# Performance work log

Hardware: AMD Instinct MI355X
Metric: run time of the kernel (lower is better)

The kernel has to match this reference:

```python
import jax, jax.numpy as jnp
import numpy as np

TOP_K = 2


def setup_inputs() -> dict:
    key = jax.random.key(0)
    ks = jax.random.split(key, 5)
    B, S, H, E, F = 4, 1024, 1024, 16, 4096
    scale = 0.02
    return {
        "input_tensor": jax.random.normal(ks[0], (B, S, H), dtype=jnp.float32),
        "Wg": scale * jax.random.normal(ks[1], (H, E), dtype=jnp.float32),
        "bg": jnp.zeros((E,), dtype=jnp.float32),
        "W1": scale * jax.random.normal(ks[2], (E, H, F), dtype=jnp.float32),
        "b1": jnp.zeros((E, F), dtype=jnp.float32),
        "W2": scale * jax.random.normal(ks[3], (E, F, H), dtype=jnp.float32),
        "b2": jnp.zeros((E, H), dtype=jnp.float32),
    }


def reference(input_tensor, Wg, bg, W1, b1, W2, b2):
    # Faithful to DualOutputMoE.forward_first_pass: the per-(b,s,k) Python loop
    # plus _weighted_sum collapses ALL token expert outputs into a single
    # [1,1,H] vector normalized by the total routing weight (= B*S).
    B, S, H = input_tensor.shape
    T = B * S
    E = Wg.shape[1]
    x = input_tensor.reshape(T, H)

    routing_scores = x @ Wg + bg                    # [T, E] (raw gate logits)
    top_v, top_i = jax.lax.top_k(routing_scores, TOP_K)
    top_w = jax.nn.softmax(top_v, axis=-1)          # per-token top-k weights

    # combine[t, e] = sum_k top_w[t, k] * 1[top_i[t, k] == e]
    combine = jnp.zeros((T, E), x.dtype).at[jnp.arange(T)[:, None], top_i].add(top_w)
    total_weight = top_w.sum()                      # matches python sum of .item()s

    def expert_step(acc, params):
        w1, bb1, w2, bb2, c = params                # c: [T] combine weights for this expert
        y = jax.nn.gelu(x @ w1 + bb1, approximate=False) @ w2 + bb2  # [T, H]
        return acc + c @ y, None

    acc0 = jnp.zeros((H,), x.dtype)
    acc, _ = jax.lax.scan(expert_step, acc0, (W1, b1, W2, b2, combine.T))
    first_output = (acc / total_weight).reshape(1, 1, H)
    return first_output
```

## Files before the change

### kernel.cpp

```cpp
#include <hip/hip_runtime.h>
#include <hip/hip_bf16.h>
#include <math.h>

typedef __bf16 bf16_t;
typedef __bf16 bf16x4 __attribute__((ext_vector_type(4)));
typedef __bf16 bf16x8 __attribute__((ext_vector_type(8)));
typedef float  f32x4  __attribute__((ext_vector_type(4)));

#define T_TOK 4096
#define H_DIM 1024
#define E_NUM 16
#define F_DIM 4096
#define CH_ROWS 128
#define CH_MAX  32

#define WS_E0     0
#define WS_E1     16384
#define WS_W0     32768
#define WS_W1     49152
#define WS_COUNTS 65536
#define WS_SUMW   65664
#define WS_XOFF   65792
#define WS_LIDX   131072
#define WS_LW     393216
#define WS_GPART  655360
#define WS_P2     655360
#define WS_G      9043968
#define WS_XE     9306112

#define AS_GLOBAL(p) ((const __attribute__((address_space(1))) void*)(p))
#define AS_LDS(p)    ((__attribute__((address_space(3))) void*)(p))

__global__ __launch_bounds__(64) void k_route(const float* __restrict__ x,
    const float* __restrict__ Wg, const float* __restrict__ bg,
    int* __restrict__ e0, int* __restrict__ e1,
    float* __restrict__ w0, float* __restrict__ w1)
{
    const int t = blockIdx.x;
    const int lane = threadIdx.x;
    const float* xr = x + (size_t)t * H_DIM;

    float s[E_NUM];
#pragma unroll
    for (int e = 0; e < E_NUM; ++e) s[e] = 0.f;

#pragma unroll
    for (int i = 0; i < 16; ++i) {
        const int h = i * 64 + lane;
        const float xv = xr[h];
        const float4* wr = (const float4*)(Wg + (size_t)h * E_NUM);
        float4 q0 = wr[0], q1 = wr[1], q2 = wr[2], q3 = wr[3];
        s[0] += xv*q0.x;  s[1] += xv*q0.y;  s[2] += xv*q0.z;  s[3] += xv*q0.w;
        s[4] += xv*q1.x;  s[5] += xv*q1.y;  s[6] += xv*q1.z;  s[7] += xv*q1.w;
        s[8] += xv*q2.x;  s[9] += xv*q2.y;  s[10]+= xv*q2.z;  s[11]+= xv*q2.w;
        s[12]+= xv*q3.x;  s[13]+= xv*q3.y;  s[14]+= xv*q3.z;  s[15]+= xv*q3.w;
    }
#pragma unroll
    for (int off = 32; off >= 1; off >>= 1) {
#pragma unroll
        for (int e = 0; e < E_NUM; ++e) s[e] += __shfl_xor(s[e], off);
    }
    if (lane == 0) {
#pragma unroll
        for (int e = 0; e < E_NUM; ++e) s[e] += bg[e];
        float b1v = -3e38f; int i1 = 0;
#pragma unroll
        for (int e = 0; e < E_NUM; ++e) { if (s[e] > b1v) { b1v = s[e]; i1 = e; } }
        float b2v = -3e38f; int i2 = 0;
#pragma unroll
        for (int e = 0; e < E_NUM; ++e) { if (e != i1 && s[e] > b2v) { b2v = s[e]; i2 = e; } }
        const float ex  = expf(b2v - b1v);
        const float inv = 1.f / (1.f + ex);
        e0[t] = i1; e1[t] = i2;
        w0[t] = inv; w1[t] = ex * inv;
    }
}

__global__ __launch_bounds__(64) void k_lists(const int* __restrict__ e0, const int* __restrict__ e1,
    const float* __restrict__ w0, const float* __restrict__ w1,
    int* __restrict__ lidx, float* __restrict__ lw,
    int* __restrict__ counts, float* __restrict__ sumw)
{
    const int e = blockIdx.x;
    const int lane = threadIdx.x;
    int cnt = 0; float sw = 0.f;
    for (int base = 0; base < T_TOK; base += 64) {
        const int t = base + lane;
        const bool m0 = (e0[t] == e);
        const bool m1 = (e1[t] == e);
        const bool m  = m0 | m1;
        const unsigned long long bal = __ballot(m);
        const int pos = cnt + __popcll(bal & ((1ull << lane) - 1ull));
        if (m) {
            const float w = m0 ? w0[t] : w1[t];
            lidx[e * T_TOK + pos] = t;
            lw[e * T_TOK + pos]   = w;
            sw += w;
        }
        cnt += __popcll(bal);
    }
#pragma unroll
    for (int off = 32; off >= 1; off >>= 1) sw += __shfl_xor(sw, off);
    if (lane == 0) { counts[e] = cnt; sumw[e] = sw; }
}

__global__ void k_scan(const int* __restrict__ counts, int* __restrict__ xoff) {
    if (threadIdx.x == 0) {
        int o = 0;
        for (int e = 0; e < E_NUM; ++e) { xoff[e] = o; o += (counts[e] + CH_ROWS - 1) & ~(CH_ROWS - 1); }
    }
}

__global__ __launch_bounds__(256) void k_gather(const float* __restrict__ x,
    const int* __restrict__ lidx, const int* __restrict__ counts,
    const int* __restrict__ xoff, bf16_t* __restrict__ Xe)
{
    const int chunk = blockIdx.x >> 2;
    const int part  = blockIdx.x & 3;
    const int e = blockIdx.y;
    const int cnt = counts[e];
    const int start = chunk * CH_ROWS;
    if (chunk && start >= cnt) return;
    const int tid = threadIdx.x;
    const size_t rbase = (size_t)xoff[e] + start;

    for (int it = part * 16; it < part * 16 + 16; ++it) {
        const int task = it * 256 + tid;
        const int rl   = task >> 7;
        const int sc   = task & 127;
        const int row  = start + rl;
        bf16x8 v8 = {};
        if (row < cnt) {
            const int tok = lidx[e * T_TOK + row];
            const int l   = (sc & 7) ^ (rl & 7);
            const int k   = (sc >> 3) * 64 + l * 8;
            const float4 a = *(const float4*)(x + (size_t)tok * H_DIM + k);
            const float4 b = *(const float4*)(x + (size_t)tok * H_DIM + k + 4);
            v8[0]=(bf16_t)a.x; v8[1]=(bf16_t)a.y; v8[2]=(bf16_t)a.z; v8[3]=(bf16_t)a.w;
            v8[4]=(bf16_t)b.x; v8[5]=(bf16_t)b.y; v8[6]=(bf16_t)b.z; v8[7]=(bf16_t)b.w;
        }
        *(bf16x8*)(Xe + (rbase + rl) * H_DIM + sc * 8) = v8;
    }
}

__global__ __launch_bounds__(256, 2) void k_expert(
    const float* __restrict__ W1, const float* __restrict__ b1,
    const bf16_t* __restrict__ Xe, const float* __restrict__ lw,
    const int* __restrict__ counts, const int* __restrict__ xoff,
    float* __restrict__ gpart)
{
    const int ftile = blockIdx.x;
    const int chunk = blockIdx.y;
    const int e     = blockIdx.z;
    const int cnt   = counts[e];
    const int start = chunk * CH_ROWS;
    if (chunk && start >= cnt) return;

    __shared__ __align__(16) bf16_t Alds[2][CH_ROWS * 64];
    __shared__ __align__(16) bf16_t Blds[2][128 * 72];
    __shared__ float w_s[CH_ROWS];
    __shared__ float b1_s[128];
    __shared__ float gred[2][128];

    const int tid  = threadIdx.x;
    const int lane = tid & 63;
    const int wid  = tid >> 6;
    const int wm   = wid & 1;
    const int wn   = wid >> 1;
    const int lr   = lane & 15;
    const int lg   = lane >> 4;

    if (tid < CH_ROWS) {
        const int r = start + tid;
        w_s[tid] = (r < cnt) ? lw[e * T_TOK + r] : 0.f;
    }
    if (tid < 128) b1_s[tid] = b1[(size_t)e * F_DIM + ftile * 128 + tid];

    f32x4 acc[4][4];
#pragma unroll
    for (int i = 0; i < 4; ++i)
#pragma unroll
        for (int j = 0; j < 4; ++j)
#pragma unroll
            for (int q = 0; q < 4; ++q) acc[i][j][q] = 0.f;

    const bf16_t* Asrc = Xe + ((size_t)xoff[e] + start) * H_DIM;
    const int bf_  = tid & 127;
    const int kh2  = tid >> 7;
    const float* W1p = W1 + (size_t)e * H_DIM * F_DIM + (size_t)ftile * 128 + bf_;

    float bvE[32], bvO[32];

#define ISSUE_A(T, BUFC) { \
    const int k0 = (T) * 64; \
    _Pragma("unroll") \
    for (int p = 0; p < 4; ++p) { \
        const int seg = wid * 4 + p; \
        const bf16_t* src = Asrc + (size_t)(seg * 8 + (lane >> 3)) * H_DIM + k0 + (lane & 7) * 8; \
        __builtin_amdgcn_global_load_lds(AS_GLOBAL(src), \
            AS_LDS((char*)&Alds[BUFC][0] + seg * 1024), 16, 0, 0); \
    } }

#define ISSUE_B(T, BV) { \
    const float* wp = W1p + (size_t)((T) * 64 + kh2 * 32) * F_DIM; \
    _Pragma("unroll") \
    for (int j = 0; j < 32; ++j) BV[j] = wp[(size_t)j * F_DIM]; }

#define WRITE_B(BUFC, BV) { \
    _Pragma("unroll") \
    for (int c = 0; c < 4; ++c) { \
        bf16x8 pk; \
        _Pragma("unroll") \
        for (int q = 0; q < 8; ++q) pk[q] = (bf16_t)BV[c * 8 + q]; \
        *(bf16x8*)&Blds[BUFC][bf_ * 72 + kh2 * 32 + c * 8] = pk; \
    } }

#define COMPUTE(BUFC) { \
    _Pragma("unroll") \
    for (int kh = 0; kh < 2; ++kh) { \
        bf16x8 af[4], bfr[4]; \
        _Pragma("unroll") \
        for (int mf = 0; mf < 4; ++mf) { \
            const int r = wm * 64 + mf * 16 + lr; \
            const int eoff = (kh * 32 + lg * 8) ^ ((r & 7) * 8); \
            af[mf] = *(const bf16x8*)&Alds[BUFC][r * 64 + eoff]; \
        } \
        _Pragma("unroll") \
        for (int nf = 0; nf < 4; ++nf) \
            bfr[nf] = *(const bf16x8*)&Blds[BUFC][(wn * 64 + nf * 16 + lr) * 72 + kh * 32 + lg * 8]; \
        _Pragma("unroll") \
        for (int mf = 0; mf < 4; ++mf) \
            _Pragma("unroll") \
            for (int nf = 0; nf < 4; ++nf) \
                acc[mf][nf] = __builtin_amdgcn_mfma_f32_16x16x32_bf16(af[mf], bfr[nf], acc[mf][nf], 0, 0, 0); \
    } }

#define SB0 __builtin_amdgcn_sched_barrier(0)

    ISSUE_A(0, 0); SB0;
    ISSUE_B(0, bvE); SB0;
    ISSUE_B(1, bvO); SB0;
    WRITE_B(0, bvE);
    asm volatile("s_waitcnt vmcnt(32) lgkmcnt(0)" ::: "memory");
    SB0; __builtin_amdgcn_s_barrier(); SB0;

#define KSTEP(T, CUR, NXT, BVISS, BVWR) { \
    if ((T) < 15) { ISSUE_A((T) + 1, NXT); } SB0; \
    if ((T) < 14) { ISSUE_B((T) + 2, BVISS); } SB0; \
    COMPUTE(CUR); \
    if ((T) < 15) { WRITE_B(NXT, BVWR); } \
    if ((T) < 14) { \
        asm volatile("s_waitcnt vmcnt(32) lgkmcnt(0)" ::: "memory"); \
    } else { \
        asm volatile("s_waitcnt vmcnt(0) lgkmcnt(0)" ::: "memory"); \
    } \
    SB0; __builtin_amdgcn_s_barrier(); SB0; }

    for (int th = 0; th < 8; ++th) {
        const int t0 = th * 2;
        KSTEP(t0,     0, 1, bvE, bvO);
        KSTEP(t0 + 1, 1, 0, bvO, bvE);
    }

    float gcol[4] = {0.f, 0.f, 0.f, 0.f};
#pragma unroll
    for (int nf = 0; nf < 4; ++nf) {
        const float bb = b1_s[wn * 64 + nf * 16 + lr];
#pragma unroll
        for (int mf = 0; mf < 4; ++mf) {
#pragma unroll
            for (int i = 0; i < 4; ++i) {
                const int row = wm * 64 + mf * 16 + lg * 4 + i;
                const float h  = acc[mf][nf][i] + bb;
                const float gl = 0.5f * h * (1.f + erff(h * 0.70710678118654752f));
                gcol[nf] += w_s[row] * gl;
            }
        }
    }
#pragma unroll
    for (int nf = 0; nf < 4; ++nf) {
        gcol[nf] += __shfl_xor(gcol[nf], 16);
        gcol[nf] += __shfl_xor(gcol[nf], 32);
    }
    if (lane < 16) {
#pragma unroll
        for (int nf = 0; nf < 4; ++nf) gred[wm][wn * 64 + nf * 16 + lane] = gcol[nf];
    }
    __syncthreads();
    if (tid < 128) {
        const float sum = gred[0][tid] + gred[1][tid];
        gpart[(size_t)(e * CH_MAX + chunk) * F_DIM + ftile * 128 + tid] = sum;
    }
#undef ISSUE_A
#undef ISSUE_B
#undef WRITE_B
#undef COMPUTE
#undef KSTEP
#undef SB0
}

__global__ __launch_bounds__(256) void k_redg(const float* __restrict__ gpart,
    const int* __restrict__ counts, float* __restrict__ g)
{
    const int e = blockIdx.y;
    const int f = blockIdx.x * 256 + threadIdx.x;
    const int nch = (counts[e] + CH_ROWS - 1) / CH_ROWS;
    float s = 0.f;
    for (int c = 0; c < nch; ++c)
        s += gpart[(size_t)(e * CH_MAX + c) * F_DIM + f];
    g[(size_t)e * F_DIM + f] = s;
}

__global__ __launch_bounds__(256) void k_out1(const float* __restrict__ g,
    const float* __restrict__ W2, float* __restrict__ p2)
{
    const int fc = blockIdx.x;
    const int e  = blockIdx.y;
    const int tid = threadIdx.x;
    __shared__ float gs[128];
    if (tid < 128) gs[tid] = g[(size_t)e * F_DIM + fc * 128 + tid];
    __syncthreads();
    const float* W2p = W2 + (size_t)e * F_DIM * H_DIM + (size_t)fc * 128 * H_DIM;
    float ax = 0.f, ay = 0.f, az = 0.f, aw = 0.f;
#pragma unroll 8
    for (int f = 0; f < 128; ++f) {
        const float gv = gs[f];
        const float4 wv = *(const float4*)(W2p + (size_t)f * H_DIM + tid * 4);
        ax += gv * wv.x; ay += gv * wv.y; az += gv * wv.z; aw += gv * wv.w;
    }
    float4 st; st.x = ax; st.y = ay; st.z = az; st.w = aw;
    *(float4*)(p2 + (size_t)(e * 32 + fc) * H_DIM + tid * 4) = st;
}

__global__ __launch_bounds__(256) void k_out2(const float* __restrict__ p2,
    const float* __restrict__ sumw, const float* __restrict__ b2, float* __restrict__ out)
{
    const int tid = threadIdx.x;
    const int hh  = tid & 31;
    const int seg = tid >> 5;
    const int h   = blockIdx.x * 32 + hh;
    float s = 0.f;
    for (int j = 0; j < 64; ++j)
        s += p2[(size_t)(seg * 64 + j) * H_DIM + h];
    __shared__ float red[8][33];
    red[seg][hh] = s;
    __syncthreads();
    if (tid < 32) {
        const int h2 = blockIdx.x * 32 + tid;
        float tot = 0.f;
#pragma unroll
        for (int q = 0; q < 8; ++q) tot += red[q][tid];
        float tw = 0.f, bias = 0.f;
#pragma unroll
        for (int e = 0; e < E_NUM; ++e) { tw += sumw[e]; bias += sumw[e] * b2[e * H_DIM + h2]; }
        out[h2] = (tot + bias) / tw;
    }
}

extern "C" void kernel_launch(void* const* d_in, const int* in_sizes, int n_in,
                              void* d_out, int out_size, void* d_ws, size_t ws_size,
                              hipStream_t stream) {
    const float* x  = (const float*)d_in[0];
    const float* Wg = (const float*)d_in[1];
    const float* bg = (const float*)d_in[2];
    const float* W1 = (const float*)d_in[3];
    const float* b1 = (const float*)d_in[4];
    const float* W2 = (const float*)d_in[5];
    const float* b2 = (const float*)d_in[6];
    float* out = (float*)d_out;

    char* ws = (char*)d_ws;
    int*    e0     = (int*)(ws + WS_E0);
    int*    e1     = (int*)(ws + WS_E1);
    float*  w0     = (float*)(ws + WS_W0);
    float*  w1     = (float*)(ws + WS_W1);
    int*    counts = (int*)(ws + WS_COUNTS);
    float*  sumw   = (float*)(ws + WS_SUMW);
    int*    xoff   = (int*)(ws + WS_XOFF);
    int*    lidx   = (int*)(ws + WS_LIDX);
    float*  lw     = (float*)(ws + WS_LW);
    float*  gpart  = (float*)(ws + WS_GPART);
    float*  g      = (float*)(ws + WS_G);
    float*  p2     = (float*)(ws + WS_P2);
    bf16_t* Xe     = (bf16_t*)(ws + WS_XE);

    k_route<<<T_TOK, 64, 0, stream>>>(x, Wg, bg, e0, e1, w0, w1);
    k_lists<<<E_NUM, 64, 0, stream>>>(e0, e1, w0, w1, lidx, lw, counts, sumw);
    k_scan<<<1, 64, 0, stream>>>(counts, xoff);
    k_gather<<<dim3(CH_MAX * 4, E_NUM), 256, 0, stream>>>(x, lidx, counts, xoff, Xe);
    k_expert<<<dim3(F_DIM / 128, CH_MAX, E_NUM), 256, 0, stream>>>(W1, b1, Xe, lw, counts, xoff, gpart);
    k_redg<<<dim3(F_DIM / 256, E_NUM), 256, 0, stream>>>(gpart, counts, g);
    k_out1<<<dim3(32, E_NUM), 256, 0, stream>>>(g, W2, p2);
    k_out2<<<32, 256, 0, stream>>>(p2, sumw, b2, out);
}
```

Baseline: 308.9 us.

## Pre-transpose W1 to swizzled bf16 tiles and stream both operands via LDS DMA

Adds a k_w1t kernel that converts each expert's W1 from fp32 into bf16 tiles laid out in 64x128 K-major blocks with an XOR swizzle. It also reorganizes the gathered Xe into contiguous tiled slabs. k_expert then loads both A and B operands with global_load_lds, replacing the strided per-thread fp32 W1 loads and register conversion, and uses a simpler double-buffered loop. The cost is an extra pass over W1 (read fp32, write bf16) plus a dependence on workspace size, which may force processing experts in batches.

Result: slower. 367.6 us (+19.0%).

```diff
diff --git a/kernel.cpp b/kernel.cpp
--- a/kernel.cpp
+++ b/kernel.cpp
@@ -27,6 +27,8 @@
 #define WS_P2     655360
 #define WS_G      9043968
 #define WS_XE     9306112
+#define WS_W1T    30277632
+#define W1T_PER_E 8388608
 
 #define AS_GLOBAL(p) ((const __attribute__((address_space(1))) void*)(p))
 #define AS_LDS(p)    ((__attribute__((address_space(3))) void*)(p))
@@ -115,49 +117,94 @@
     const int* __restrict__ lidx, const int* __restrict__ counts,
     const int* __restrict__ xoff, bf16_t* __restrict__ Xe)
 {
-    const int chunk = blockIdx.x >> 2;
-    const int part  = blockIdx.x & 3;
+    const int chunk = blockIdx.x >> 1;
+    const int part  = blockIdx.x & 1;
     const int e = blockIdx.y;
     const int cnt = counts[e];
     const int start = chunk * CH_ROWS;
     if (chunk && start >= cnt) return;
     const int tid = threadIdx.x;
-    const size_t rbase = (size_t)xoff[e] + start;
-
-    for (int it = part * 16; it < part * 16 + 16; ++it) {
-        const int task = it * 256 + tid;
-        const int rl   = task >> 7;
-        const int sc   = task & 127;
+    const size_t base = ((size_t)(xoff[e] >> 7) + chunk) * 131072;
+
+    for (int it = 0; it < 32; ++it) {
+        const int u    = part * 8192 + it * 256 + tid;
+        const int kt   = u >> 10;
+        const int wi   = u & 1023;
+        const int rl   = wi >> 3;
+        const int c    = wi & 7;
         const int row  = start + rl;
         bf16x8 v8 = {};
         if (row < cnt) {
             const int tok = lidx[e * T_TOK + row];
-            const int l   = (sc & 7) ^ (rl & 7);
-            const int k   = (sc >> 3) * 64 + l * 8;
+            const int cp  = c ^ (rl & 7);
+            const int k   = kt * 64 + cp * 8;
             const float4 a = *(const float4*)(x + (size_t)tok * H_DIM + k);
             const float4 b = *(const float4*)(x + (size_t)tok * H_DIM + k + 4);
             v8[0]=(bf16_t)a.x; v8[1]=(bf16_t)a.y; v8[2]=(bf16_t)a.z; v8[3]=(bf16_t)a.w;
             v8[4]=(bf16_t)b.x; v8[5]=(bf16_t)b.y; v8[6]=(bf16_t)b.z; v8[7]=(bf16_t)b.w;
         }
-        *(bf16x8*)(Xe + (rbase + rl) * H_DIM + sc * 8) = v8;
+        *(bf16x8*)(Xe + base + (size_t)kt * 8192 + rl * 64 + c * 8) = v8;
+    }
+}
+
+__global__ __launch_bounds__(512, 1) void k_w1t(const float* __restrict__ W1,
+    bf16_t* __restrict__ W1T, int ebase)
+{
+    const int kt = blockIdx.x;
+    const int fq = blockIdx.y;
+    const int ge = blockIdx.z;
+    const int e  = ebase + ge;
+    const int tid = threadIdx.x;
+
+    __shared__ bf16_t S[64][1024];
+
+    const float* src = W1 + (size_t)e * H_DIM * F_DIM + (size_t)(kt * 64) * F_DIM + fq * 1024;
+    for (int it = 0; it < 32; ++it) {
+        const int u   = it * 512 + tid;
+        const int row = u >> 8;
+        const int c4  = u & 255;
+        const float4 v = *(const float4*)(src + (size_t)row * F_DIM + c4 * 4);
+        bf16x4 b4; b4[0]=(bf16_t)v.x; b4[1]=(bf16_t)v.y; b4[2]=(bf16_t)v.z; b4[3]=(bf16_t)v.w;
+        *(bf16x4*)&S[row][c4 * 4] = b4;
+    }
+    __syncthreads();
+
+#pragma unroll
+    for (int ot = 0; ot < 2; ++ot) {
+        const int orow = ot * 512 + tid;
+        const int ftl  = orow >> 7;
+        const int f    = orow & 127;
+        const int fg   = ftl * 128 + f;
+        bf16_t kv[64];
+#pragma unroll
+        for (int k = 0; k < 64; ++k) kv[k] = S[k][fg];
+        bf16_t* dst = W1T + ((((size_t)ge * 32 + (fq * 8 + ftl)) * 16 + kt) * 8192) + f * 64;
+#pragma unroll
+        for (int j = 0; j < 8; ++j) {
+            bf16x8 pk;
+#pragma unroll
+            for (int q = 0; q < 8; ++q) pk[q] = kv[j * 8 + q];
+            *(bf16x8*)&dst[((j ^ (f & 7)) * 8)] = pk;
+        }
     }
 }
 
 __global__ __launch_bounds__(256, 2) void k_expert(
-    const float* __restrict__ W1, const float* __restrict__ b1,
+    const bf16_t* __restrict__ W1T, const float* __restrict__ b1,
     const bf16_t* __restrict__ Xe, const float* __restrict__ lw,
     const int* __restrict__ counts, const int* __restrict__ xoff,
-    float* __restrict__ gpart)
+    float* __restrict__ gpart, int ebase)
 {
     const int ftile = blockIdx.x;
     const int chunk = blockIdx.y;
-    const int e     = blockIdx.z;
+    const int ge    = blockIdx.z;
+    const int e     = ebase + ge;
     const int cnt   = counts[e];
     const int start = chunk * CH_ROWS;
     if (chunk && start >= cnt) return;
 
-    __shared__ __align__(16) bf16_t Alds[2][CH_ROWS * 64];
-    __shared__ __align__(16) bf16_t Blds[2][128 * 72];
+    __shared__ __align__(16) bf16_t Alds[2][8192];
+    __shared__ __align__(16) bf16_t Blds[2][8192];
     __shared__ float w_s[CH_ROWS];
     __shared__ float b1_s[128];
     __shared__ float gred[2][128];
@@ -184,50 +231,33 @@
 #pragma unroll
             for (int q = 0; q < 4; ++q) acc[i][j][q] = 0.f;
 
-    const bf16_t* Asrc = Xe + ((size_t)xoff[e] + start) * H_DIM;
-    const int bf_  = tid & 127;
-    const int kh2  = tid >> 7;
-    const float* W1p = W1 + (size_t)e * H_DIM * F_DIM + (size_t)ftile * 128 + bf_;
-
-    float bvE[32], bvO[32];
-
-#define ISSUE_A(T, BUFC) { \
-    const int k0 = (T) * 64; \
+    const bf16_t* XeSlab = Xe + ((size_t)(xoff[e] >> 7) + chunk) * 131072;
+    const bf16_t* W1Slab = W1T + (((size_t)ge * 32 + ftile) * 16) * 8192;
+
+#define STAGE(T, BUF) { \
+    const bf16_t* sa = XeSlab + (size_t)(T) * 8192; \
+    const bf16_t* sb = W1Slab + (size_t)(T) * 8192; \
     _Pragma("unroll") \
     for (int p = 0; p < 4; ++p) { \
-        const int seg = wid * 4 + p; \
-        const bf16_t* src = Asrc + (size_t)(seg * 8 + (lane >> 3)) * H_DIM + k0 + (lane & 7) * 8; \
-        __builtin_amdgcn_global_load_lds(AS_GLOBAL(src), \
-            AS_LDS((char*)&Alds[BUFC][0] + seg * 1024), 16, 0, 0); \
+        const int off = p * 2048 + wid * 512; \
+        __builtin_amdgcn_global_load_lds(AS_GLOBAL(sa + off + lane * 8), AS_LDS(&Alds[BUF][off]), 16, 0, 0); \
+        __builtin_amdgcn_global_load_lds(AS_GLOBAL(sb + off + lane * 8), AS_LDS(&Blds[BUF][off]), 16, 0, 0); \
     } }
 
-#define ISSUE_B(T, BV) { \
-    const float* wp = W1p + (size_t)((T) * 64 + kh2 * 32) * F_DIM; \
-    _Pragma("unroll") \
-    for (int j = 0; j < 32; ++j) BV[j] = wp[(size_t)j * F_DIM]; }
-
-#define WRITE_B(BUFC, BV) { \
-    _Pragma("unroll") \
-    for (int c = 0; c < 4; ++c) { \
-        bf16x8 pk; \
-        _Pragma("unroll") \
-        for (int q = 0; q < 8; ++q) pk[q] = (bf16_t)BV[c * 8 + q]; \
-        *(bf16x8*)&Blds[BUFC][bf_ * 72 + kh2 * 32 + c * 8] = pk; \
-    } }
-
-#define COMPUTE(BUFC) { \
+#define COMPUTE(BUF) { \
     _Pragma("unroll") \
     for (int kh = 0; kh < 2; ++kh) { \
         bf16x8 af[4], bfr[4]; \
         _Pragma("unroll") \
         for (int mf = 0; mf < 4; ++mf) { \
             const int r = wm * 64 + mf * 16 + lr; \
-            const int eoff = (kh * 32 + lg * 8) ^ ((r & 7) * 8); \
-            af[mf] = *(const bf16x8*)&Alds[BUFC][r * 64 + eoff]; \
+            af[mf] = *(const bf16x8*)&Alds[BUF][r * 64 + (((kh << 2) | lg) ^ (r & 7)) * 8]; \
         } \
         _Pragma("unroll") \
-        for (int nf = 0; nf < 4; ++nf) \
-            bfr[nf] = *(const bf16x8*)&Blds[BUFC][(wn * 64 + nf * 16 + lr) * 72 + kh * 32 + lg * 8]; \
+        for (int nf = 0; nf < 4; ++nf) { \
+            const int f = wn * 64 + nf * 16 + lr; \
+            bfr[nf] = *(const bf16x8*)&Blds[BUF][f * 64 + (((kh << 2) | lg) ^ (f & 7)) * 8]; \
+        } \
         _Pragma("unroll") \
         for (int mf = 0; mf < 4; ++mf) \
             _Pragma("unroll") \
@@ -235,32 +265,20 @@
                 acc[mf][nf] = __builtin_amdgcn_mfma_f32_16x16x32_bf16(af[mf], bfr[nf], acc[mf][nf], 0, 0, 0); \
     } }
 
-#define SB0 __builtin_amdgcn_sched_barrier(0)
-
-    ISSUE_A(0, 0); SB0;
-    ISSUE_B(0, bvE); SB0;
-    ISSUE_B(1, bvO); SB0;
-    WRITE_B(0, bvE);
-    asm volatile("s_waitcnt vmcnt(32) lgkmcnt(0)" ::: "memory");
-    SB0; __builtin_amdgcn_s_barrier(); SB0;
-
-#define KSTEP(T, CUR, NXT, BVISS, BVWR) { \
-    if ((T) < 15) { ISSUE_A((T) + 1, NXT); } SB0; \
-    if ((T) < 14) { ISSUE_B((T) + 2, BVISS); } SB0; \
-    COMPUTE(CUR); \
-    if ((T) < 15) { WRITE_B(NXT, BVWR); } \
-    if ((T) < 14) { \
-        asm volatile("s_waitcnt vmcnt(32) lgkmcnt(0)" ::: "memory"); \
-    } else { \
-        asm volatile("s_waitcnt vmcnt(0) lgkmcnt(0)" ::: "memory"); \
-    } \
-    SB0; __builtin_amdgcn_s_barrier(); SB0; }
-
-    for (int th = 0; th < 8; ++th) {
-        const int t0 = th * 2;
-        KSTEP(t0,     0, 1, bvE, bvO);
-        KSTEP(t0 + 1, 1, 0, bvO, bvE);
-    }
+    STAGE(0, 0);
+    __syncthreads();
+
+    int cur = 0;
+#pragma unroll 2
+    for (int t = 0; t < 16; ++t) {
+        if (t < 15) { STAGE(t + 1, cur ^ 1); }
+        __builtin_amdgcn_sched_barrier(0);
+        COMPUTE(cur);
+        __syncthreads();
+        cur ^= 1;
+    }
+#undef STAGE
+#undef COMPUTE
 
     float gcol[4] = {0.f, 0.f, 0.f, 0.f};
 #pragma unroll
@@ -291,12 +309,6 @@
         const float sum = gred[0][tid] + gred[1][tid];
         gpart[(size_t)(e * CH_MAX + chunk) * F_DIM + ftile * 128 + tid] = sum;
     }
-#undef ISSUE_A
-#undef ISSUE_B
-#undef WRITE_B
-#undef COMPUTE
-#undef KSTEP
-#undef SB0
 }
 
 __global__ __launch_bounds__(256) void k_redg(const float* __restrict__ gpart,
@@ -383,12 +395,24 @@
     float*  g      = (float*)(ws + WS_G);
     float*  p2     = (float*)(ws + WS_P2);
     bf16_t* Xe     = (bf16_t*)(ws + WS_XE);
+    bf16_t* W1T    = (bf16_t*)(ws + WS_W1T);
+
+    int cap = 1;
+    if (ws_size > (size_t)WS_W1T + (size_t)W1T_PER_E) {
+        size_t c = (ws_size - (size_t)WS_W1T) / (size_t)W1T_PER_E;
+        cap = (c >= 16) ? 16 : (int)c;
+        if (cap < 1) cap = 1;
+    }
 
     k_route<<<T_TOK, 64, 0, stream>>>(x, Wg, bg, e0, e1, w0, w1);
     k_lists<<<E_NUM, 64, 0, stream>>>(e0, e1, w0, w1, lidx, lw, counts, sumw);
     k_scan<<<1, 64, 0, stream>>>(counts, xoff);
-    k_gather<<<dim3(CH_MAX * 4, E_NUM), 256, 0, stream>>>(x, lidx, counts, xoff, Xe);
-    k_expert<<<dim3(F_DIM / 128, CH_MAX, E_NUM), 256, 0, stream>>>(W1, b1, Xe, lw, counts, xoff, gpart);
+    k_gather<<<dim3(CH_MAX * 2, E_NUM), 256, 0, stream>>>(x, lidx, counts, xoff, Xe);
+    for (int eb = 0; eb < E_NUM; eb += cap) {
+        const int gN = (E_NUM - eb < cap) ? (E_NUM - eb) : cap;
+        k_w1t<<<dim3(16, 4, gN), 512, 0, stream>>>(W1, W1T, eb);
+        k_expert<<<dim3(32, CH_MAX, gN), 256, 0, stream>>>(W1T, b1, Xe, lw, counts, xoff, gpart, eb);
+    }
     k_redg<<<dim3(F_DIM / 256, E_NUM), 256, 0, stream>>>(gpart, counts, g);
     k_out1<<<dim3(32, E_NUM), 256, 0, stream>>>(g, W2, p2);
     k_out2<<<32, 256, 0, stream>>>(p2, sumw, b2, out);
```
